# Optimization experiments

Hardware: AMD Instinct MI355X
Metric: run time of the kernel (lower is better)

The kernel has to match this reference:

```python
import jax, jax.numpy as jnp
import numpy as np
from jax import lax

GAMMA = 0.01   # SoftDTWLossPyTorch(gamma=0.01)
INF = 1e10     # large finite sentinel for out-of-band DP cells (safe exp underflow)
C1 = 0.01 ** 2 # piqa SSIM constants, value_range=1
C2 = 0.03 ** 2


def _gauss_kernel(size=11, sigma=1.5):
    g = np.exp(-0.5 * ((np.arange(size) - (size - 1) / 2.0) / sigma) ** 2)
    g = g / g.sum()
    return jnp.asarray(np.outer(g, g).astype(np.float32))


def _blur(x, k2d):
    # depthwise valid Gaussian filter; x: [P, C, H, W]
    P, C, H, W = x.shape
    y = lax.conv_general_dilated(x.reshape(P * C, 1, H, W), k2d[None, None], (1, 1), 'VALID')
    return y.reshape(P, C, y.shape[-2], y.shape[-1])


def _ssim_pairs(x, y):
    # x, y: [P, 3, H, W] in [0,1]; returns per-pair mean SSIM [P] (piqa SSIM, reduction='none')
    k2d = _gauss_kernel()
    mu_x = _blur(x, k2d)
    mu_y = _blur(y, k2d)
    sxx = _blur(x * x, k2d) - mu_x ** 2
    syy = _blur(y * y, k2d) - mu_y ** 2
    sxy = _blur(x * y, k2d) - mu_x * mu_y
    num = (2.0 * mu_x * mu_y + C1) * (2.0 * sxy + C2)
    den = (mu_x ** 2 + mu_y ** 2 + C1) * (sxx + syy + C2)
    return (num / den).mean(axis=(1, 2, 3))


def _soft_dtw(x, y, gamma=GAMMA):
    # squared-euclidean soft-DTW for every (b, s) pair, wavefront over anti-diagonals
    # x: [B, T], y: [S, T] -> [B, S]
    B, T = x.shape
    S = y.shape[0]
    D = (x[:, None, :, None] - y[None, :, None, :]) ** 2  # [B, S, T, T]
    ii = jnp.arange(T)
    kk = jnp.arange(2 * T - 1)
    jj = kk[:, None] - ii[None, :]              # column index of cell i on diag k
    valid = (jj >= 0) & (jj < T)                # [2T-1, T]
    Dd = jnp.moveaxis(D[:, :, ii[None, :], jnp.clip(jj, 0, T - 1)], 2, 0)  # [2T-1, B, S, T]
    i0 = ii == 0

    def softmin3(a, b, c):
        m = jnp.minimum(jnp.minimum(a, b), c)
        return m - gamma * jnp.log(
            jnp.exp(-(a - m) / gamma) + jnp.exp(-(b - m) / gamma) + jnp.exp(-(c - m) / gamma))

    def step(carry, xs):
        r2, r1 = carry                     # diagonals k-2, k-1, each [B, S, T]
        d, v, k = xs
        pad = jnp.full(r1.shape[:-1] + (1,), INF, r1.dtype)
        r1s = jnp.concatenate([pad, r1[..., :-1]], axis=-1)  # R[i-1, j]
        r2s = jnp.concatenate([pad, r2[..., :-1]], axis=-1)  # R[i-1, j-1]
        sm = softmin3(r2s, r1s, r1)        # r1 itself is R[i, j-1]
        sm = jnp.where((k == 0) & i0, 0.0, sm)  # base cell R[0,0] = D[0,0]
        r = jnp.where(v, d + sm, INF)
        return (r1, r), None

    init = (jnp.full((B, S, T), INF, jnp.float32), jnp.full((B, S, T), INF, jnp.float32))
    (_, rf), _ = lax.scan(step, init, (Dd, valid, kk))
    return rf[..., -1]  # R[T-1, T-1]


def _forward(input, samples, img, sample_img, output, labels):
    B = input.shape[0]
    S = samples.shape[0]
    # all (sample, batch-image) pairs for SSIM; ssim(sample_img[i], img[b])
    X = jnp.broadcast_to(sample_img[None], (B,) + sample_img.shape).reshape((B * S,) + sample_img.shape[1:])
    Y = jnp.broadcast_to(img[:, None], (B, S) + img.shape[1:]).reshape((B * S,) + img.shape[1:])
    ssim = _ssim_pairs(X, Y).reshape(B, S)
    m0 = (1.0 - ssim) * 10.0
    m1 = _soft_dtw(input, samples) / 500.0
    per_b = ((m0 + m1) / 2.0).mean(axis=1)   # metrics.mean(dim=2).mean(dim=1)
    metric_sum = per_b.sum()
    # torch BCELoss with log clamped at -100
    ln = jnp.clip(jnp.log(output), -100.0, None)
    ln1 = jnp.clip(jnp.log1p(-output), -100.0, None)
    bce = -jnp.mean(labels * ln + (1.0 - labels) * ln1)
    loss = bce + metric_sum / 10.0
    return loss, bce, metric_sum


def setup_inputs() -> dict:
    key = jax.random.key(0)
    k1, k2, k3, k4, k5, k6 = jax.random.split(key, 6)
    B, S, T, H, W = 32, 8, 256, 128, 128
    return {
        'input': jax.random.normal(k1, (B, T), dtype=jnp.float32),
        'samples': jax.random.normal(k2, (S, T), dtype=jnp.float32),
        'img': jax.random.uniform(k3, (B, 3, H, W), dtype=jnp.float32),
        'sample_img': jax.random.uniform(k4, (S, 3, H, W), dtype=jnp.float32),
        'output': jax.random.uniform(k5, (B, 1), dtype=jnp.float32) * 0.98 + 0.01,
        'labels': (jax.random.uniform(k6, (B, 1)) < 0.5).astype(jnp.float32),
    }


def reference(input, samples, img, sample_img, output, labels):
    return _forward(input, samples, img, sample_img, output, labels)
```

## Files before the change

### kernel.cpp

```cpp
#include <hip/hip_runtime.h>
#include <math.h>

#define IW 128
#define OW 118
#define OWP 120
#define NPIX (IW*IW)
#define MOW (OW*OW)
#define NS 8
#define NB 32
#define NIMG 40
#define TT 256
#define SC1 0.0001f
#define SC2 0.0009f
#define NBAND 4
#define BROWS 30

__device__ __forceinline__ unsigned bfp(float x) {
    unsigned u = __float_as_uint(x);
    return (u + 0x7fffu + ((u >> 16) & 1u)) >> 16;
}
__device__ __forceinline__ float bflo(unsigned w) { return __uint_as_float(w << 16); }
__device__ __forceinline__ float bfhi(unsigned w) { return __uint_as_float(w & 0xffff0000u); }

__device__ __forceinline__ void gauss_regs(float* g) {
    float s = 0.f;
#pragma unroll
    for (int i = 0; i < 11; ++i) { float t = (i - 5) * (1.0f / 1.5f); g[i] = expf(-0.5f * t * t); s += g[i]; }
    float inv = 1.f / s;
#pragma unroll
    for (int i = 0; i < 11; ++i) g[i] *= inv;
}

__global__ __launch_bounds__(256) void k_mom(const float* __restrict__ img,
        const float* __restrict__ simg, unsigned* __restrict__ MOM) {
    __shared__ float sR[NIMG * IW + 8];
    __shared__ float sHv[NIMG * OWP];
    __shared__ float sHs[NIMG * OWP];
    int cb = blockIdx.x, im = blockIdx.y;
    int ch = cb >> 2, band = cb & 3;
    int r0 = band * BROWS;
    int nrows = (118 - r0 < BROWS) ? (118 - r0) : BROWS;
    int in_rows = nrows + 10, irm1 = in_rows - 1;
    const float* src = (im < NS) ? (simg + (size_t)(im * 3 + ch) * NPIX)
                                 : (img  + (size_t)((im - NS) * 3 + ch) * NPIX);
    float g[11]; gauss_regs(g);
    int t = threadIdx.x;
    for (int i4 = t; i4 < in_rows * (IW / 4); i4 += 256) {
        int r = i4 >> 5, c4 = i4 & 31;
        ((float4*)sR)[(r << 5) + c4] = ((const float4*)(src + (size_t)(r0 + r) * IW))[c4];
    }
    __syncthreads();
    {
        int cg = t & 31, tr = t >> 5;
        for (int rb = 0; rb < in_rows; rb += 8) {
            int r = rb + tr;
            if (r < in_rows && cg < 30) {
                const float* p = sR + r * IW + cg * 4;
                float4 A = *(const float4*)p, B = *(const float4*)(p + 4), C = *(const float4*)(p + 8);
                float2 D = *(const float2*)(p + 12);
                float w[14] = {A.x,A.y,A.z,A.w,B.x,B.y,B.z,B.w,C.x,C.y,C.z,C.w,D.x,D.y};
                float a0=0,a1=0,a2=0,a3=0,q0=0,q1=0,q2=0,q3=0;
#pragma unroll
                for (int k = 0; k < 11; ++k) {
                    float gk = g[k];
                    a0=fmaf(gk,w[k],a0); a1=fmaf(gk,w[k+1],a1); a2=fmaf(gk,w[k+2],a2); a3=fmaf(gk,w[k+3],a3);
                    q0=fmaf(gk,w[k]*w[k],q0); q1=fmaf(gk,w[k+1]*w[k+1],q1);
                    q2=fmaf(gk,w[k+2]*w[k+2],q2); q3=fmaf(gk,w[k+3]*w[k+3],q3);
                }
                *(float4*)(sHv + r * OWP + cg * 4) = make_float4(a0,a1,a2,a3);
                *(float4*)(sHs + r * OWP + cg * 4) = make_float4(q0,q1,q2,q3);
            }
        }
    }
    __syncthreads();
    unsigned* out = MOM + (size_t)(im * 3 + ch) * MOW;
    int c = t & 127, half = t >> 7;
    for (int sb = 0; sb < 8; sb += 2) {
        int rr = (sb + half) * 4;
        if (c < 118 && rr < nrows) {
            float va0=0,va1=0,va2=0,va3=0,vq0=0,vq1=0,vq2=0,vq3=0;
#pragma unroll
            for (int k = 0; k < 11; ++k) {
                float gk = g[k];
                int k0=rr+k, k1=k0+1, k2=k0+2, k3=k0+3;
                k0=k0<irm1?k0:irm1; k1=k1<irm1?k1:irm1; k2=k2<irm1?k2:irm1; k3=k3<irm1?k3:irm1;
                va0=fmaf(gk,sHv[k0*OWP+c],va0); va1=fmaf(gk,sHv[k1*OWP+c],va1);
                va2=fmaf(gk,sHv[k2*OWP+c],va2); va3=fmaf(gk,sHv[k3*OWP+c],va3);
                vq0=fmaf(gk,sHs[k0*OWP+c],vq0); vq1=fmaf(gk,sHs[k1*OWP+c],vq1);
                vq2=fmaf(gk,sHs[k2*OWP+c],vq2); vq3=fmaf(gk,sHs[k3*OWP+c],vq3);
            }
            float ua[4]={va0,va1,va2,va3}, uq[4]={vq0,vq1,vq2,vq3};
#pragma unroll
            for (int i = 0; i < 4; ++i) {
                if (rr + i < nrows) {
                    float m = ua[i], var = uq[i] - m * m;
                    out[(size_t)(r0 + rr + i) * OW + c] = bfp(m) | (bfp(var) << 16);
                }
            }
        }
    }
}

__global__ __launch_bounds__(256) void k_pairdtw(const float* __restrict__ img,
        const float* __restrict__ simg, const unsigned* __restrict__ MOM,
        float* __restrict__ SP, const float* __restrict__ input,
        const float* __restrict__ samples, float* __restrict__ dtw) {
    __shared__ float SM[NIMG * IW + 8 + NIMG * OWP];
    int bid = blockIdx.x;
    int t = threadIdx.x;
    if (bid < 64) {
        const float FINF = 1e10f;
        int w = t >> 6, l = t & 63;
        int pair = bid * 4 + w;
        int b = pair >> 3, s = pair & 7;
        float* sY = SM + (w << 8);
        *(float4*)(sY + l * 4) = *(const float4*)(samples + s * TT + l * 4);
        float4 xv = *(const float4*)(input + b * TT + l * 4);
        float x0 = xv.x, x1 = xv.y, x2 = xv.z, x3 = xv.w;
        __syncthreads();
        float left0 = FINF, left1 = FINF, left2 = FINF, left3 = FINF;
        float bot0 = FINF, bot1 = FINF, bot1p = FINF;
        for (int m = 0; m < 191; ++m) {
            float t0  = __shfl_up(bot0, 1);
            float t1  = __shfl_up(bot1, 1);
            float tdl = __shfl_up(bot1p, 1);
            if (l == 0) { t0 = FINF; t1 = FINF; tdl = FINF; }
            int c = m - l;
            if (0 <= c && c < 128) {
                float2 yv = *(const float2*)(sY + 2 * c);
                float y0 = yv.x, y1 = yv.y;
                bot1p = bot1;
                float up0 = t0, up1 = t1, dg = tdl, v0, v1;
#define CELLH(x_, y_, a_, b_, c_, out_) { float d_ = (x_) - (y_); \
                out_ = fmaf(d_, d_, fminf(fminf((a_), (b_)), (c_))); }
                CELLH(x0, y0, dg, up0, left0, v0);
                if ((l | c) == 0) { float d0 = x0 - y0; v0 = d0 * d0; }
                CELLH(x0, y1, up0, up1, v0, v1);
                dg = left0; left0 = v1; up0 = v0; up1 = v1;
                CELLH(x1, y0, dg, up0, left1, v0);
                CELLH(x1, y1, up0, up1, v0, v1);
                dg = left1; left1 = v1; up0 = v0; up1 = v1;
                CELLH(x2, y0, dg, up0, left2, v0);
                CELLH(x2, y1, up0, up1, v0, v1);
                dg = left2; left2 = v1; up0 = v0; up1 = v1;
                CELLH(x3, y0, dg, up0, left3, v0);
                CELLH(x3, y1, up0, up1, v0, v1);
                left3 = v1; up0 = v0; up1 = v1;
                bot0 = up0; bot1 = up1;
            }
        }
        if (l == 63) dtw[pair] = bot1;
        return;
    }
    int pid = bid - 64;
    int xcd = pid & 7;
    int idx = pid >> 3;
    int q = (idx >= 288) ? 3 : (idx >= 192) ? 2 : (idx >= 96) ? 1 : 0;
    int rem = idx - q * 96;
    int b = xcd * 4 + q;
    int s = rem & 7;
    int cb = rem >> 3;
    int ch = cb >> 2, band = cb & 3;
    int r0 = band * BROWS;
    int nrows = (118 - r0 < BROWS) ? (118 - r0) : BROWS;
    int in_rows = nrows + 10, irm1 = in_rows - 1;
    float* sP = SM;
    float* sH = SM + NIMG * IW + 8;
    const float* xs = simg + (size_t)(s * 3 + ch) * NPIX;
    const float* ys = img  + (size_t)(b * 3 + ch) * NPIX;
    float g[11]; gauss_regs(g);
    for (int i4 = t; i4 < in_rows * (IW / 4); i4 += 256) {
        int r = i4 >> 5, c4 = i4 & 31;
        float4 xv = ((const float4*)(xs + (size_t)(r0 + r) * IW))[c4];
        float4 yv = ((const float4*)(ys + (size_t)(r0 + r) * IW))[c4];
        ((float4*)sP)[(r << 5) + c4] = make_float4(xv.x*yv.x, xv.y*yv.y, xv.z*yv.z, xv.w*yv.w);
    }
    __syncthreads();
    {
        int cg = t & 31, tr = t >> 5;
        for (int rb = 0; rb < in_rows; rb += 8) {
            int r = rb + tr;
            if (r < in_rows && cg < 30) {
                const float* p = sP + r * IW + cg * 4;
                float4 A = *(const float4*)p, B = *(const float4*)(p + 4), C = *(const float4*)(p + 8);
                float2 D = *(const float2*)(p + 12);
                float w[14] = {A.x,A.y,A.z,A.w,B.x,B.y,B.z,B.w,C.x,C.y,C.z,C.w,D.x,D.y};
                float o0=0,o1=0,o2=0,o3=0;
#pragma unroll
                for (int k = 0; k < 11; ++k) {
                    float gk = g[k];
                    o0=fmaf(gk,w[k],o0); o1=fmaf(gk,w[k+1],o1); o2=fmaf(gk,w[k+2],o2); o3=fmaf(gk,w[k+3],o3);
                }
                *(float4*)(sH + r * OWP + cg * 4) = make_float4(o0,o1,o2,o3);
            }
        }
    }
    __syncthreads();
    const unsigned* Mx = MOM + (size_t)(s * 3 + ch) * MOW;
    const unsigned* My = MOM + (size_t)((NS + b) * 3 + ch) * MOW;
    float lsum = 0.f;
    int c = t & 127, half = t >> 7;
    for (int sb = 0; sb < 8; sb += 2) {
        int rr = (sb + half) * 4;
        if (c < 118 && rr < nrows) {
            float a0=0,a1=0,a2=0,a3=0;
#pragma unroll
            for (int k = 0; k < 11; ++k) {
                float gk = g[k];
                int k0=rr+k, k1=k0+1, k2=k0+2, k3=k0+3;
                k0=k0<irm1?k0:irm1; k1=k1<irm1?k1:irm1; k2=k2<irm1?k2:irm1; k3=k3<irm1?k3:irm1;
                a0=fmaf(gk,sH[k0*OWP+c],a0); a1=fmaf(gk,sH[k1*OWP+c],a1);
                a2=fmaf(gk,sH[k2*OWP+c],a2); a3=fmaf(gk,sH[k3*OWP+c],a3);
            }
            float bxy[4] = {a0,a1,a2,a3};
#pragma unroll
            for (int i = 0; i < 4; ++i) {
                size_t gidx = (size_t)(r0 + rr + i) * OW + c;
                unsigned wx = Mx[gidx], wy = My[gidx];
                float ux = bflo(wx), sxx = bfhi(wx);
                float uy = bflo(wy), syy = bfhi(wy);
                float sxy = bxy[i] - ux * uy;
                float num = (2.f * ux * uy + SC1) * (2.f * sxy + SC2);
                float den = (ux * ux + uy * uy + SC1) * (sxx + syy + SC2);
                lsum += (rr + i < nrows) ? num / den : 0.f;
            }
        }
    }
#pragma unroll
    for (int off = 32; off > 0; off >>= 1) lsum += __shfl_down(lsum, off);
    if ((t & 63) == 0) sP[t >> 6] = lsum;
    __syncthreads();
    int pair = b * 8 + s;
    if (t == 0) SP[((pair * 3) + ch) * NBAND + band] = sP[0] + sP[1] + sP[2] + sP[3];
}

__global__ __launch_bounds__(256) void k_final(const float* __restrict__ SP,
        const float* __restrict__ DTW, const float* __restrict__ outp,
        const float* __restrict__ lab, float* __restrict__ out) {
    __shared__ float redm[4], redb[4];
    int t = threadIdx.x;
    float ssum = 0.f;
#pragma unroll
    for (int i = 0; i < 3 * NBAND; ++i) ssum += SP[t * 3 * NBAND + i];
    float ssim = ssum * (1.0f / 41772.0f);
    float m0 = (1.f - ssim) * 10.f;
    float m1 = DTW[t] * (1.f / 500.f);
    float m = (m0 + m1) * 0.5f;
    float bt = 0.f;
    if (t < 32) {
        float o = outp[t], l = lab[t];
        float ln  = fmaxf(logf(o), -100.f);
        float ln1 = fmaxf(log1pf(-o), -100.f);
        bt = l * ln + (1.f - l) * ln1;
    }
#pragma unroll
    for (int off = 32; off > 0; off >>= 1) { m += __shfl_down(m, off); bt += __shfl_down(bt, off); }
    if ((t & 63) == 0) { redm[t >> 6] = m; redb[t >> 6] = bt; }
    __syncthreads();
    if (t == 0) {
        float msum = redm[0] + redm[1] + redm[2] + redm[3];
        float bsum = redb[0] + redb[1] + redb[2] + redb[3];
        float metric_sum = msum * 0.125f;
        float bce = -bsum * (1.f / 32.f);
        out[0] = bce + metric_sum * 0.1f;
        out[1] = bce;
        out[2] = metric_sum;
    }
}

extern "C" void kernel_launch(void* const* d_in, const int* in_sizes, int n_in,
                              void* d_out, int out_size, void* d_ws, size_t ws_size,
                              hipStream_t stream) {
    const float* input   = (const float*)d_in[0];
    const float* samples = (const float*)d_in[1];
    const float* img     = (const float*)d_in[2];
    const float* simg    = (const float*)d_in[3];
    const float* outp    = (const float*)d_in[4];
    const float* lab     = (const float*)d_in[5];
    float* out = (float*)d_out;
    unsigned* MOM = (unsigned*)d_ws;
    float* SP  = (float*)d_ws + (size_t)NIMG * 3 * MOW;
    float* DTW = SP + 256 * 3 * NBAND;

    k_mom    <<<dim3(12, 40),  dim3(256), 0, stream>>>(img, simg, MOM);
    k_pairdtw<<<dim3(64 + 3072), dim3(256), 0, stream>>>(img, simg, MOM, SP, input, samples, DTW);
    k_final  <<<dim3(1),       dim3(256), 0, stream>>>(SP, DTW, outp, lab, out);
}
```

Baseline: 118.2 us.

## Overlap soft-DTW with moment blur kernel and vectorize vertical blur passes

Moves the soft-DTW wavefront blocks out of the large pair kernel and into the moment-computation kernel, so the long serial DTW chains run alongside the moment blur rather than at the start of the 3072-block pair launch. The vertical blur passes in both the moment and pair kernels are rewritten so each thread handles a 4-column float4 strip per row, replacing per-column scalar shared-memory loads and clamped row indices. This frees the pair kernel from DTW tail latency and cuts shared-memory instruction count. In exchange, the moment kernel's shared-memory footprint grows, and per-thread work in the vertical pass is less balanced.

```diff
diff --git a/kernel.cpp b/kernel.cpp
--- a/kernel.cpp
+++ b/kernel.cpp
@@ -31,81 +31,11 @@
     for (int i = 0; i < 11; ++i) g[i] *= inv;
 }
 
-__global__ __launch_bounds__(256) void k_mom(const float* __restrict__ img,
-        const float* __restrict__ simg, unsigned* __restrict__ MOM) {
-    __shared__ float sR[NIMG * IW + 8];
-    __shared__ float sHv[NIMG * OWP];
-    __shared__ float sHs[NIMG * OWP];
-    int cb = blockIdx.x, im = blockIdx.y;
-    int ch = cb >> 2, band = cb & 3;
-    int r0 = band * BROWS;
-    int nrows = (118 - r0 < BROWS) ? (118 - r0) : BROWS;
-    int in_rows = nrows + 10, irm1 = in_rows - 1;
-    const float* src = (im < NS) ? (simg + (size_t)(im * 3 + ch) * NPIX)
-                                 : (img  + (size_t)((im - NS) * 3 + ch) * NPIX);
-    float g[11]; gauss_regs(g);
-    int t = threadIdx.x;
-    for (int i4 = t; i4 < in_rows * (IW / 4); i4 += 256) {
-        int r = i4 >> 5, c4 = i4 & 31;
-        ((float4*)sR)[(r << 5) + c4] = ((const float4*)(src + (size_t)(r0 + r) * IW))[c4];
-    }
-    __syncthreads();
-    {
-        int cg = t & 31, tr = t >> 5;
-        for (int rb = 0; rb < in_rows; rb += 8) {
-            int r = rb + tr;
-            if (r < in_rows && cg < 30) {
-                const float* p = sR + r * IW + cg * 4;
-                float4 A = *(const float4*)p, B = *(const float4*)(p + 4), C = *(const float4*)(p + 8);
-                float2 D = *(const float2*)(p + 12);
-                float w[14] = {A.x,A.y,A.z,A.w,B.x,B.y,B.z,B.w,C.x,C.y,C.z,C.w,D.x,D.y};
-                float a0=0,a1=0,a2=0,a3=0,q0=0,q1=0,q2=0,q3=0;
-#pragma unroll
-                for (int k = 0; k < 11; ++k) {
-                    float gk = g[k];
-                    a0=fmaf(gk,w[k],a0); a1=fmaf(gk,w[k+1],a1); a2=fmaf(gk,w[k+2],a2); a3=fmaf(gk,w[k+3],a3);
-                    q0=fmaf(gk,w[k]*w[k],q0); q1=fmaf(gk,w[k+1]*w[k+1],q1);
-                    q2=fmaf(gk,w[k+2]*w[k+2],q2); q3=fmaf(gk,w[k+3]*w[k+3],q3);
-                }
-                *(float4*)(sHv + r * OWP + cg * 4) = make_float4(a0,a1,a2,a3);
-                *(float4*)(sHs + r * OWP + cg * 4) = make_float4(q0,q1,q2,q3);
-            }
-        }
-    }
-    __syncthreads();
-    unsigned* out = MOM + (size_t)(im * 3 + ch) * MOW;
-    int c = t & 127, half = t >> 7;
-    for (int sb = 0; sb < 8; sb += 2) {
-        int rr = (sb + half) * 4;
-        if (c < 118 && rr < nrows) {
-            float va0=0,va1=0,va2=0,va3=0,vq0=0,vq1=0,vq2=0,vq3=0;
-#pragma unroll
-            for (int k = 0; k < 11; ++k) {
-                float gk = g[k];
-                int k0=rr+k, k1=k0+1, k2=k0+2, k3=k0+3;
-                k0=k0<irm1?k0:irm1; k1=k1<irm1?k1:irm1; k2=k2<irm1?k2:irm1; k3=k3<irm1?k3:irm1;
-                va0=fmaf(gk,sHv[k0*OWP+c],va0); va1=fmaf(gk,sHv[k1*OWP+c],va1);
-                va2=fmaf(gk,sHv[k2*OWP+c],va2); va3=fmaf(gk,sHv[k3*OWP+c],va3);
-                vq0=fmaf(gk,sHs[k0*OWP+c],vq0); vq1=fmaf(gk,sHs[k1*OWP+c],vq1);
-                vq2=fmaf(gk,sHs[k2*OWP+c],vq2); vq3=fmaf(gk,sHs[k3*OWP+c],vq3);
-            }
-            float ua[4]={va0,va1,va2,va3}, uq[4]={vq0,vq1,vq2,vq3};
-#pragma unroll
-            for (int i = 0; i < 4; ++i) {
-                if (rr + i < nrows) {
-                    float m = ua[i], var = uq[i] - m * m;
-                    out[(size_t)(r0 + rr + i) * OW + c] = bfp(m) | (bfp(var) << 16);
-                }
-            }
-        }
-    }
-}
-
-__global__ __launch_bounds__(256) void k_pairdtw(const float* __restrict__ img,
-        const float* __restrict__ simg, const unsigned* __restrict__ MOM,
-        float* __restrict__ SP, const float* __restrict__ input,
-        const float* __restrict__ samples, float* __restrict__ dtw) {
-    __shared__ float SM[NIMG * IW + 8 + NIMG * OWP];
+__global__ __launch_bounds__(256) void k_dtwmom(const float* __restrict__ img,
+        const float* __restrict__ simg, unsigned* __restrict__ MOM,
+        const float* __restrict__ input, const float* __restrict__ samples,
+        float* __restrict__ dtw) {
+    __shared__ float SM[NIMG * IW + 8 + 2 * NIMG * OWP];
     int bid = blockIdx.x;
     int t = threadIdx.x;
     if (bid < 64) {
@@ -152,7 +82,78 @@
         if (l == 63) dtw[pair] = bot1;
         return;
     }
-    int pid = bid - 64;
+    int id = bid - 64;
+    int im = id % 40, cb = id / 40;
+    int ch = cb >> 2, band = cb & 3;
+    int r0 = band * BROWS;
+    int nrows = (118 - r0 < BROWS) ? (118 - r0) : BROWS;
+    int in_rows = nrows + 10;
+    const float* src = (im < NS) ? (simg + (size_t)(im * 3 + ch) * NPIX)
+                                 : (img  + (size_t)((im - NS) * 3 + ch) * NPIX);
+    float* sR  = SM;
+    float* sHv = SM + NIMG * IW + 8;
+    float* sHs = sHv + NIMG * OWP;
+    float g[11]; gauss_regs(g);
+    for (int i4 = t; i4 < in_rows * (IW / 4); i4 += 256) {
+        int r = i4 >> 5, c4 = i4 & 31;
+        ((float4*)sR)[(r << 5) + c4] = ((const float4*)(src + (size_t)(r0 + r) * IW))[c4];
+    }
+    __syncthreads();
+    {
+        int cg = t & 31, tr = t >> 5;
+        for (int rb = 0; rb < in_rows; rb += 8) {
+            int r = rb + tr;
+            if (r < in_rows && cg < 30) {
+                const float* p = sR + r * IW + cg * 4;
+                float4 A = *(const float4*)p, B = *(const float4*)(p + 4), C = *(const float4*)(p + 8);
+                float2 D = *(const float2*)(p + 12);
+                float w[14] = {A.x,A.y,A.z,A.w,B.x,B.y,B.z,B.w,C.x,C.y,C.z,C.w,D.x,D.y};
+                float a0=0,a1=0,a2=0,a3=0,q0=0,q1=0,q2=0,q3=0;
+#pragma unroll
+                for (int k = 0; k < 11; ++k) {
+                    float gk = g[k];
+                    a0=fmaf(gk,w[k],a0); a1=fmaf(gk,w[k+1],a1); a2=fmaf(gk,w[k+2],a2); a3=fmaf(gk,w[k+3],a3);
+                    q0=fmaf(gk,w[k]*w[k],q0); q1=fmaf(gk,w[k+1]*w[k+1],q1);
+                    q2=fmaf(gk,w[k+2]*w[k+2],q2); q3=fmaf(gk,w[k+3]*w[k+3],q3);
+                }
+                *(float4*)(sHv + r * OWP + cg * 4) = make_float4(a0,a1,a2,a3);
+                *(float4*)(sHs + r * OWP + cg * 4) = make_float4(q0,q1,q2,q3);
+            }
+        }
+    }
+    __syncthreads();
+    unsigned* out = MOM + (size_t)(im * 3 + ch) * MOW;
+    for (int qi = t; qi < nrows * 30; qi += 256) {
+        int r = qi / 30, cq = qi - r * 30;
+        float4 av = make_float4(0,0,0,0), aq = make_float4(0,0,0,0);
+#pragma unroll
+        for (int k = 0; k < 11; ++k) {
+            float gk = g[k];
+            float4 hv = ((const float4*)(sHv + (r + k) * OWP))[cq];
+            float4 hq = ((const float4*)(sHs + (r + k) * OWP))[cq];
+            av.x=fmaf(gk,hv.x,av.x); av.y=fmaf(gk,hv.y,av.y); av.z=fmaf(gk,hv.z,av.z); av.w=fmaf(gk,hv.w,av.w);
+            aq.x=fmaf(gk,hq.x,aq.x); aq.y=fmaf(gk,hq.y,aq.y); aq.z=fmaf(gk,hq.z,aq.z); aq.w=fmaf(gk,hq.w,aq.w);
+        }
+        float ua[4] = {av.x, av.y, av.z, av.w};
+        float uq[4] = {aq.x, aq.y, aq.z, aq.w};
+        int c0 = cq * 4;
+#pragma unroll
+        for (int i = 0; i < 4; ++i) {
+            int c = c0 + i;
+            if (c < 118) {
+                float m = ua[i], var = uq[i] - m * m;
+                out[(size_t)(r0 + r) * OW + c] = bfp(m) | (bfp(var) << 16);
+            }
+        }
+    }
+}
+
+__global__ __launch_bounds__(256) void k_pair(const float* __restrict__ img,
+        const float* __restrict__ simg, const unsigned* __restrict__ MOM,
+        float* __restrict__ SP) {
+    __shared__ float SM[NIMG * IW + 8 + NIMG * OWP];
+    int pid = blockIdx.x;
+    int t = threadIdx.x;
     int xcd = pid & 7;
     int idx = pid >> 3;
     int q = (idx >= 288) ? 3 : (idx >= 192) ? 2 : (idx >= 96) ? 1 : 0;
@@ -163,7 +164,7 @@
     int ch = cb >> 2, band = cb & 3;
     int r0 = band * BROWS;
     int nrows = (118 - r0 < BROWS) ? (118 - r0) : BROWS;
-    int in_rows = nrows + 10, irm1 = in_rows - 1;
+    int in_rows = nrows + 10;
     float* sP = SM;
     float* sH = SM + NIMG * IW + 8;
     const float* xs = simg + (size_t)(s * 3 + ch) * NPIX;
@@ -199,30 +200,29 @@
     const unsigned* Mx = MOM + (size_t)(s * 3 + ch) * MOW;
     const unsigned* My = MOM + (size_t)((NS + b) * 3 + ch) * MOW;
     float lsum = 0.f;
-    int c = t & 127, half = t >> 7;
-    for (int sb = 0; sb < 8; sb += 2) {
-        int rr = (sb + half) * 4;
-        if (c < 118 && rr < nrows) {
-            float a0=0,a1=0,a2=0,a3=0;
-#pragma unroll
-            for (int k = 0; k < 11; ++k) {
-                float gk = g[k];
-                int k0=rr+k, k1=k0+1, k2=k0+2, k3=k0+3;
-                k0=k0<irm1?k0:irm1; k1=k1<irm1?k1:irm1; k2=k2<irm1?k2:irm1; k3=k3<irm1?k3:irm1;
-                a0=fmaf(gk,sH[k0*OWP+c],a0); a1=fmaf(gk,sH[k1*OWP+c],a1);
-                a2=fmaf(gk,sH[k2*OWP+c],a2); a3=fmaf(gk,sH[k3*OWP+c],a3);
-            }
-            float bxy[4] = {a0,a1,a2,a3};
-#pragma unroll
-            for (int i = 0; i < 4; ++i) {
-                size_t gidx = (size_t)(r0 + rr + i) * OW + c;
-                unsigned wx = Mx[gidx], wy = My[gidx];
+    for (int qi = t; qi < nrows * 30; qi += 256) {
+        int r = qi / 30, cq = qi - r * 30;
+        float4 acc = make_float4(0,0,0,0);
+#pragma unroll
+        for (int k = 0; k < 11; ++k) {
+            float gk = g[k];
+            float4 h = ((const float4*)(sH + (r + k) * OWP))[cq];
+            acc.x=fmaf(gk,h.x,acc.x); acc.y=fmaf(gk,h.y,acc.y); acc.z=fmaf(gk,h.z,acc.z); acc.w=fmaf(gk,h.w,acc.w);
+        }
+        float bxy[4] = {acc.x, acc.y, acc.z, acc.w};
+        int c0 = cq * 4;
+        size_t grow = (size_t)(r0 + r) * OW;
+#pragma unroll
+        for (int i = 0; i < 4; ++i) {
+            int c = c0 + i;
+            if (c < 118) {
+                unsigned wx = Mx[grow + c], wy = My[grow + c];
                 float ux = bflo(wx), sxx = bfhi(wx);
                 float uy = bflo(wy), syy = bfhi(wy);
                 float sxy = bxy[i] - ux * uy;
                 float num = (2.f * ux * uy + SC1) * (2.f * sxy + SC2);
                 float den = (ux * ux + uy * uy + SC1) * (sxx + syy + SC2);
-                lsum += (rr + i < nrows) ? num / den : 0.f;
+                lsum += num / den;
             }
         }
     }
@@ -282,7 +282,7 @@
     float* SP  = (float*)d_ws + (size_t)NIMG * 3 * MOW;
     float* DTW = SP + 256 * 3 * NBAND;
 
-    k_mom    <<<dim3(12, 40),  dim3(256), 0, stream>>>(img, simg, MOM);
-    k_pairdtw<<<dim3(64 + 3072), dim3(256), 0, stream>>>(img, simg, MOM, SP, input, samples, DTW);
-    k_final  <<<dim3(1),       dim3(256), 0, stream>>>(SP, DTW, outp, lab, out);
-}
+    k_dtwmom<<<dim3(64 + 480), dim3(256), 0, stream>>>(img, simg, MOM, input, samples, DTW);
+    k_pair  <<<dim3(3072),     dim3(256), 0, stream>>>(img, simg, MOM, SP);
+    k_final <<<dim3(1),        dim3(256), 0, stream>>>(SP, DTW, outp, lab, out);
+}
```

After: 153.0 us. 29.4% more time.
